# Optimization experiments

Hardware: AMD Instinct MI355X
Metric: run time of the kernel (lower is better)

Reference implementation:

```python
import jax, jax.numpy as jnp
import numpy as np

N = 50000      # nodes
E = 200000     # edges (before self-loops)
D_IN = 256
HID = 128
NEG_SLOPE = 0.2
BN_EPS = 1e-5


def _lin(k, fan_in, fan_out):
    return jax.random.normal(k, (fan_in, fan_out), jnp.float32) / np.float32(np.sqrt(fan_in))


def setup_inputs() -> dict:
    key = jax.random.key(0)
    ks = jax.random.split(key, 40)
    d = {}
    d['x'] = jax.random.normal(ks[0], (N, D_IN), jnp.float32)
    d['edge_index'] = jax.random.randint(ks[1], (2, E), 0, N, dtype=jnp.int32)
    # GAT layer 1: 256 -> 128, heads=4 (concat -> 512)
    d['W1'] = _lin(ks[2], D_IN, 4 * HID)
    d['asrc1'] = jax.random.normal(ks[3], (4, HID), jnp.float32) * 0.1
    d['adst1'] = jax.random.normal(ks[4], (4, HID), jnp.float32) * 0.1
    d['b1'] = jnp.zeros((4 * HID,), jnp.float32)
    d['g1'] = jax.random.uniform(ks[5], (4 * HID,), jnp.float32, 0.5, 1.5)
    d['be1'] = jax.random.normal(ks[6], (4 * HID,), jnp.float32) * 0.1
    d['m1'] = jax.random.normal(ks[7], (4 * HID,), jnp.float32) * 0.1
    d['v1'] = jax.random.uniform(ks[8], (4 * HID,), jnp.float32, 0.5, 1.5)
    # GAT layer 2: 512 -> 128, heads=4 (concat -> 512)
    d['W2'] = _lin(ks[9], 4 * HID, 4 * HID)
    d['asrc2'] = jax.random.normal(ks[10], (4, HID), jnp.float32) * 0.1
    d['adst2'] = jax.random.normal(ks[11], (4, HID), jnp.float32) * 0.1
    d['b2'] = jnp.zeros((4 * HID,), jnp.float32)
    d['g2'] = jax.random.uniform(ks[12], (4 * HID,), jnp.float32, 0.5, 1.5)
    d['be2'] = jax.random.normal(ks[13], (4 * HID,), jnp.float32) * 0.1
    d['m2'] = jax.random.normal(ks[14], (4 * HID,), jnp.float32) * 0.1
    d['v2'] = jax.random.uniform(ks[15], (4 * HID,), jnp.float32, 0.5, 1.5)
    # GAT layer 3: 512 -> 128, heads=1
    d['W3'] = _lin(ks[16], 4 * HID, HID)
    d['asrc3'] = jax.random.normal(ks[17], (1, HID), jnp.float32) * 0.1
    d['adst3'] = jax.random.normal(ks[18], (1, HID), jnp.float32) * 0.1
    d['b3'] = jnp.zeros((HID,), jnp.float32)
    d['g3'] = jax.random.uniform(ks[19], (HID,), jnp.float32, 0.5, 1.5)
    d['be3'] = jax.random.normal(ks[20], (HID,), jnp.float32) * 0.1
    d['m3'] = jax.random.normal(ks[21], (HID,), jnp.float32) * 0.1
    d['v3'] = jax.random.uniform(ks[22], (HID,), jnp.float32, 0.5, 1.5)
    # classifier head: 128 -> 64 -> 10
    d['Wc1'] = _lin(ks[23], HID, HID // 2)
    d['bc1'] = jnp.zeros((HID // 2,), jnp.float32)
    d['Wc2'] = _lin(ks[24], HID // 2, 10)
    d['bc2'] = jnp.zeros((10,), jnp.float32)
    return d


def _gat_layer(h, src, dst, W, asrc, adst, b, heads, ch):
    # PyG GATConv (eval mode): linear -> per-head scores -> segment softmax over dst -> aggregate
    xp = (h @ W).reshape(-1, heads, ch)                 # [N, H, C]
    e_src = (xp * asrc[None]).sum(-1)                   # [N, H]
    e_dst = (xp * adst[None]).sum(-1)                   # [N, H]
    e = jax.nn.leaky_relu(e_src[src] + e_dst[dst], NEG_SLOPE)  # [E', H]
    m = jax.lax.stop_gradient(jax.ops.segment_max(e, dst, num_segments=N))
    w = jnp.exp(e - m[dst])
    s = jax.ops.segment_sum(w, dst, num_segments=N)     # [N, H]
    alpha = w / (s[dst] + 1e-16)                        # [E', H]
    out = jax.ops.segment_sum(alpha[:, :, None] * xp[src], dst, num_segments=N)  # [N, H, C]
    return out.reshape(-1, heads * ch) + b


def _bn_relu(h, g, be, mu, var):
    return jax.nn.relu((h - mu) * jax.lax.rsqrt(var + BN_EPS) * g + be)


def reference(x, edge_index,
              W1, asrc1, adst1, b1, g1, be1, m1, v1,
              W2, asrc2, adst2, b2, g2, be2, m2, v2,
              W3, asrc3, adst3, b3, g3, be3, m3, v3,
              Wc1, bc1, Wc2, bc2):
    loop = jnp.arange(N, dtype=edge_index.dtype)
    src = jnp.concatenate([edge_index[0], loop])        # GATConv adds self-loops
    dst = jnp.concatenate([edge_index[1], loop])
    h = _bn_relu(_gat_layer(x, src, dst, W1, asrc1, adst1, b1, 4, HID), g1, be1, m1, v1)
    h = _bn_relu(_gat_layer(h, src, dst, W2, asrc2, adst2, b2, 4, HID), g2, be2, m2, v2)
    h = _bn_relu(_gat_layer(h, src, dst, W3, asrc3, adst3, b3, 1, HID), g3, be3, m3, v3)
    E_GNN = h                                           # [N, 128]
    logits = jax.nn.relu(E_GNN @ Wc1 + bc1) @ Wc2 + bc2 # [N, 10]
    P_GNN = jax.nn.softmax(logits, axis=-1)
    return (E_GNN, P_GNN)
```

## Files before the change

### kernel.cpp

```cpp
#include <hip/hip_runtime.h>
#include <math.h>

#define N_NODES 50000
#define N_EDGES 200000
#define NEG_SLOPE 0.2f
#define BN_EPS 1e-5f

#define SCAN_ELEMS 1024
#define SCAN_NB ((N_NODES + SCAN_ELEMS - 1) / SCAN_ELEMS)

typedef __attribute__((ext_vector_type(4))) float f32x4;
typedef __attribute__((ext_vector_type(8))) short bf16x8;
typedef __attribute__((ext_vector_type(8))) ushort u16x8;
typedef __attribute__((ext_vector_type(2))) ushort u16x2;

__device__ __forceinline__ ushort f2bf(float x) {
    unsigned u = __float_as_uint(x);
    u += 0x7FFFu + ((u >> 16) & 1u);
    return (ushort)(u >> 16);
}
__device__ __forceinline__ float bf2f(ushort u) {
    return __uint_as_float(((unsigned)u) << 16);
}

__global__ void k_init(int* cnt, int* off) {
    int i = blockIdx.x * blockDim.x + threadIdx.x;
    if (i < N_NODES) { cnt[i] = 1; off[i] = 1; }
}

__global__ void k_count(const int* __restrict__ ei, int* cnt) {
    int e = blockIdx.x * blockDim.x + threadIdx.x;
    if (e < N_EDGES) atomicAdd(&cnt[ei[N_EDGES + e]], 1);
}

__global__ __launch_bounds__(256) void k_scan1(const int* __restrict__ cnt,
                                               int* __restrict__ incl,
                                               int* __restrict__ partials) {
    __shared__ int sh[256];
    const int t = threadIdx.x;
    const int base = blockIdx.x * SCAN_ELEMS + t * 4;
    int v0 = 0, v1 = 0, v2 = 0, v3 = 0;
    if (base + 3 < N_NODES) {
        int4 lv = *reinterpret_cast<const int4*>(&cnt[base]);
        v0 = lv.x; v1 = lv.y; v2 = lv.z; v3 = lv.w;
    } else {
        if (base + 0 < N_NODES) v0 = cnt[base + 0];
        if (base + 1 < N_NODES) v1 = cnt[base + 1];
        if (base + 2 < N_NODES) v2 = cnt[base + 2];
        if (base + 3 < N_NODES) v3 = cnt[base + 3];
    }
    const int s1 = v0 + v1, s2 = s1 + v2, s3 = s2 + v3;
    sh[t] = s3;
    __syncthreads();
#pragma unroll
    for (int off = 1; off < 256; off <<= 1) {
        int x = (t >= off) ? sh[t - off] : 0;
        __syncthreads();
        sh[t] += x;
        __syncthreads();
    }
    const int excl = sh[t] - s3;
    if (base + 0 < N_NODES) incl[base + 0] = excl + v0;
    if (base + 1 < N_NODES) incl[base + 1] = excl + s1;
    if (base + 2 < N_NODES) incl[base + 2] = excl + s2;
    if (base + 3 < N_NODES) incl[base + 3] = excl + s3;
    if (t == 255) partials[blockIdx.x] = sh[255];
}

__global__ void k_scan2(const int* __restrict__ partials, int* __restrict__ pofs) {
    if (threadIdx.x == 0) {
        int s = 0;
        for (int b = 0; b < SCAN_NB; ++b) { pofs[b] = s; s += partials[b]; }
    }
}

__global__ void k_scan3(const int* __restrict__ incl, const int* __restrict__ pofs,
                        int* __restrict__ row_ptr) {
    int i = blockIdx.x * blockDim.x + threadIdx.x;
    if (i < N_NODES) row_ptr[i + 1] = incl[i] + pofs[i >> 10];
    if (i == 0) row_ptr[0] = 0;
}

__global__ void k_self(const int* __restrict__ row_ptr, int* colb) {
    int n = blockIdx.x * blockDim.x + threadIdx.x;
    if (n < N_NODES) colb[row_ptr[n]] = n;
}

__global__ void k_scatter(const int* __restrict__ ei, const int* __restrict__ row_ptr,
                          int* off, int* colb) {
    int e = blockIdx.x * blockDim.x + threadIdx.x;
    if (e < N_EDGES) {
        int dst = ei[N_EDGES + e];
        int p = atomicAdd(&off[dst], 1);
        colb[row_ptr[dst] + p] = ei[e];
    }
}

__global__ void k_cvt(const float* __restrict__ in, ushort* __restrict__ out, int n4) {
    int i = blockIdx.x * blockDim.x + threadIdx.x;
    if (i < n4) {
        float4 v = reinterpret_cast<const float4*>(in)[i];
        ushort4 o;
        o.x = f2bf(v.x); o.y = f2bf(v.y); o.z = f2bf(v.z); o.w = f2bf(v.w);
        reinterpret_cast<ushort4*>(out)[i] = o;
    }
}

__global__ void k_wt(const float* __restrict__ W, ushort* __restrict__ Wt, int K, int N) {
    int idx = blockIdx.x * blockDim.x + threadIdx.x;
    if (idx < K * N) {
        int n = idx / K, k = idx - n * K;
        Wt[idx] = f2bf(W[(size_t)k * N + n]);
    }
}

__global__ __launch_bounds__(512) void k_gemm256(const ushort* __restrict__ A,
                                                 const ushort* __restrict__ Bt,
                                                 ushort* __restrict__ Cb,
                                                 const float* __restrict__ asrc,
                                                 const float* __restrict__ adst,
                                                 float* __restrict__ es,
                                                 float* __restrict__ ed,
                                                 int M, int K) {
    constexpr int N = 512;
    __shared__ __align__(16) ushort As[128 * 32];
    __shared__ __align__(16) ushort Bs[256 * 32];
    __shared__ float sles[4][128];
    __shared__ float sled[4][128];
    const int tid = threadIdx.x;
    const int wid = tid >> 6, lane = tid & 63;
    const int wm = wid >> 2, wn = wid & 3;

    const int nwg = gridDim.x;
    const int q = nwg >> 3, r = nwg & 7;
    const int xcd = blockIdx.x & 7, bidx = blockIdx.x >> 3;
    const int wg = ((xcd < r) ? xcd * (q + 1) : r * (q + 1) + (xcd - r) * q) + bidx;
    const int row0 = (wg >> 1) * 128;
    const int by = wg & 1;
    const int col0 = by * 256;

    const int sub = lane >> 2;
    const int kcol = (lane & 3) * 8;

    const ushort* gPtr[3];
    ushort* lBase[3];
#pragma unroll
    for (int c = 0; c < 3; ++c) {
        int chunk = wid * 3 + c;
        if (chunk < 8) {
            int ar = row0 + chunk * 16 + sub;
            if (ar > M - 1) ar = M - 1;
            gPtr[c] = A + (size_t)ar * K + kcol;
            lBase[c] = As + chunk * 512;
        } else {
            int bc = chunk - 8;
            gPtr[c] = Bt + (size_t)(col0 + bc * 16 + sub) * K + kcol;
            lBase[c] = Bs + bc * 512;
        }
    }

    const int afr = (wm * 64 + (lane & 15)) * 32 + (lane >> 4) * 8;
    const int bfr = (wn * 64 + (lane & 15)) * 32 + (lane >> 4) * 8;

    f32x4 acc[4][4] = {};

    for (int k0 = 0; k0 < K; k0 += 32) {
#pragma unroll
        for (int c = 0; c < 3; ++c) {
            __builtin_amdgcn_global_load_lds(
                (const __attribute__((address_space(1))) unsigned*)(gPtr[c] + k0),
                (__attribute__((address_space(3))) unsigned*)lBase[c], 16, 0, 0);
        }
        __syncthreads();

        bf16x8 af[4], bg[4];
#pragma unroll
        for (int m = 0; m < 4; ++m)
            af[m] = *reinterpret_cast<const bf16x8*>(&As[afr + m * 16 * 32]);
#pragma unroll
        for (int n = 0; n < 4; ++n)
            bg[n] = *reinterpret_cast<const bf16x8*>(&Bs[bfr + n * 16 * 32]);
#pragma unroll
        for (int m = 0; m < 4; ++m)
#pragma unroll
            for (int n = 0; n < 4; ++n)
                acc[m][n] = __builtin_amdgcn_mfma_f32_16x16x32_bf16(af[m], bg[n], acc[m][n], 0, 0, 0);
        __syncthreads();
    }

    const int crow = row0 + wm * 64 + (lane >> 4) * 4;
    const int ccol = col0 + wn * 64 + (lane & 15);
#pragma unroll
    for (int m = 0; m < 4; ++m) {
#pragma unroll
        for (int j = 0; j < 4; ++j) {
            int rr = crow + m * 16 + j;
            if (rr < M) {
#pragma unroll
                for (int n = 0; n < 4; ++n)
                    Cb[(size_t)rr * N + ccol + n * 16] = f2bf(acc[m][n][j]);
            }
        }
    }

    const int head = by * 2 + (wn >> 1);
    float as_c[4], ad_c[4];
#pragma unroll
    for (int n = 0; n < 4; ++n) {
        int cl = (wn & 1) * 64 + n * 16 + (lane & 15);
        as_c[n] = asrc[head * 128 + cl];
        ad_c[n] = adst[head * 128 + cl];
    }
#pragma unroll
    for (int m = 0; m < 4; ++m) {
#pragma unroll
        for (int j = 0; j < 4; ++j) {
            float ps = acc[m][0][j] * as_c[0] + acc[m][1][j] * as_c[1] +
                       acc[m][2][j] * as_c[2] + acc[m][3][j] * as_c[3];
            float pd = acc[m][0][j] * ad_c[0] + acc[m][1][j] * ad_c[1] +
                       acc[m][2][j] * ad_c[2] + acc[m][3][j] * ad_c[3];
#pragma unroll
            for (int o = 1; o < 16; o <<= 1) {
                ps += __shfl_xor(ps, o);
                pd += __shfl_xor(pd, o);
            }
            if ((lane & 15) == 0) {
                int rl = wm * 64 + (lane >> 4) * 4 + m * 16 + j;
                sles[wn][rl] = ps;
                sled[wn][rl] = pd;
            }
        }
    }
    __syncthreads();
    if (tid < 256) {
        const int hl = tid >> 7;
        const int rl = tid & 127;
        const int rr = row0 + rl;
        if (rr < M) {
            es[(size_t)rr * 4 + by * 2 + hl] = sles[2 * hl][rl] + sles[2 * hl + 1][rl];
            ed[(size_t)rr * 4 + by * 2 + hl] = sled[2 * hl][rl] + sled[2 * hl + 1][rl];
        }
    }
}

__global__ __launch_bounds__(256) void k_gemm_bf16(const ushort* __restrict__ A,
                                                   const ushort* __restrict__ Bt,
                                                   ushort* __restrict__ Cb,
                                                   const float* __restrict__ asrc,
                                                   const float* __restrict__ adst,
                                                   float* __restrict__ es,
                                                   float* __restrict__ ed,
                                                   int M, int K, int N) {
    __shared__ __align__(16) ushort As[128 * 32];
    __shared__ __align__(16) ushort Bs[128 * 32];
    __shared__ float sles[2][128];
    __shared__ float sled[2][128];
    const int tid = threadIdx.x;
    const int wid = tid >> 6, lane = tid & 63;
    const int wm = wid >> 1, wn = wid & 1;
    const int row0 = blockIdx.x * 128, col0 = blockIdx.y * 128;
    const int H = N >> 7;

    const int c0 = wid * 2;
    const int sub = lane >> 2;
    const int kcol = (lane & 3) * 8;

    int ar0 = row0 + c0 * 16 + sub;      if (ar0 > M - 1) ar0 = M - 1;
    int ar1 = row0 + c0 * 16 + 16 + sub; if (ar1 > M - 1) ar1 = M - 1;
    const size_t gA0 = (size_t)ar0 * K + kcol;
    const size_t gA1 = (size_t)ar1 * K + kcol;
    const size_t gB0 = (size_t)(col0 + c0 * 16 + sub) * K + kcol;
    const size_t gB1 = gB0 + (size_t)16 * K;
    ushort* lA0 = As + c0 * 512;
    ushort* lA1 = lA0 + 512;
    ushort* lB0 = Bs + c0 * 512;
    ushort* lB1 = lB0 + 512;

    const int afr = (wm * 64 + (lane & 15)) * 32 + (lane >> 4) * 8;
    const int bfr = (wn * 64 + (lane & 15)) * 32 + (lane >> 4) * 8;

    f32x4 acc[4][4] = {};

    for (int k0 = 0; k0 < K; k0 += 32) {
        __builtin_amdgcn_global_load_lds(
            (const __attribute__((address_space(1))) unsigned*)(A + gA0 + k0),
            (__attribute__((address_space(3))) unsigned*)lA0, 16, 0, 0);
        __builtin_amdgcn_global_load_lds(
            (const __attribute__((address_space(1))) unsigned*)(A + gA1 + k0),
            (__attribute__((address_space(3))) unsigned*)lA1, 16, 0, 0);
        __builtin_amdgcn_global_load_lds(
            (const __attribute__((address_space(1))) unsigned*)(Bt + gB0 + k0),
            (__attribute__((address_space(3))) unsigned*)lB0, 16, 0, 0);
        __builtin_amdgcn_global_load_lds(
            (const __attribute__((address_space(1))) unsigned*)(Bt + gB1 + k0),
            (__attribute__((address_space(3))) unsigned*)lB1, 16, 0, 0);
        __syncthreads();

        bf16x8 af[4], bg[4];
#pragma unroll
        for (int m = 0; m < 4; ++m)
            af[m] = *reinterpret_cast<const bf16x8*>(&As[afr + m * 16 * 32]);
#pragma unroll
        for (int n = 0; n < 4; ++n)
            bg[n] = *reinterpret_cast<const bf16x8*>(&Bs[bfr + n * 16 * 32]);
#pragma unroll
        for (int m = 0; m < 4; ++m)
#pragma unroll
            for (int n = 0; n < 4; ++n)
                acc[m][n] = __builtin_amdgcn_mfma_f32_16x16x32_bf16(af[m], bg[n], acc[m][n], 0, 0, 0);
        __syncthreads();
    }

    const int crow = row0 + wm * 64 + (lane >> 4) * 4;
    const int ccol = col0 + wn * 64 + (lane & 15);
#pragma unroll
    for (int m = 0; m < 4; ++m) {
#pragma unroll
        for (int j = 0; j < 4; ++j) {
            int r = crow + m * 16 + j;
            if (r < M) {
#pragma unroll
                for (int n = 0; n < 4; ++n)
                    Cb[(size_t)r * N + ccol + n * 16] = f2bf(acc[m][n][j]);
            }
        }
    }

    float as_c[4], ad_c[4];
#pragma unroll
    for (int n = 0; n < 4; ++n) {
        int cl = wn * 64 + n * 16 + (lane & 15);
        as_c[n] = asrc[blockIdx.y * 128 + cl];
        ad_c[n] = adst[blockIdx.y * 128 + cl];
    }
#pragma unroll
    for (int m = 0; m < 4; ++m) {
#pragma unroll
        for (int j = 0; j < 4; ++j) {
            float ps = acc[m][0][j] * as_c[0] + acc[m][1][j] * as_c[1] +
                       acc[m][2][j] * as_c[2] + acc[m][3][j] * as_c[3];
            float pd = acc[m][0][j] * ad_c[0] + acc[m][1][j] * ad_c[1] +
                       acc[m][2][j] * ad_c[2] + acc[m][3][j] * ad_c[3];
#pragma unroll
            for (int o = 1; o < 16; o <<= 1) {
                ps += __shfl_xor(ps, o);
                pd += __shfl_xor(pd, o);
            }
            if ((lane & 15) == 0) {
                int rl = wm * 64 + (lane >> 4) * 4 + m * 16 + j;
                sles[wn][rl] = ps;
                sled[wn][rl] = pd;
            }
        }
    }
    __syncthreads();
    if (tid < 128) {
        int r = row0 + tid;
        if (r < M) {
            es[(size_t)r * H + blockIdx.y] = sles[0][tid] + sles[1][tid];
            ed[(size_t)r * H + blockIdx.y] = sled[0][tid] + sled[1][tid];
        }
    }
}

template <int H, bool BF16OUT>
__global__ __launch_bounds__(64) void k_agg(
    const ushort* __restrict__ xpb, const float* __restrict__ es, const float* __restrict__ ed,
    const int* __restrict__ row_ptr, const int* __restrict__ colb,
    const float* __restrict__ bias, const float* __restrict__ gg, const float* __restrict__ be,
    const float* __restrict__ mu, const float* __restrict__ var, void* __restrict__ outv) {
    constexpr int HC = H * 128;
    constexpr int CPT = HC / 64;
    constexpr int CHUNK = 128;
    constexpr int GS = (H == 4) ? 16 : 64;
    __shared__ int s_src[CHUNK];
    __shared__ float s_w[CHUNK][H];
    const int n = blockIdx.x;
    const int lane = threadIdx.x;
    const int g = (H == 4) ? (lane >> 4) : 0;
    const int gl = (H == 4) ? (lane & 15) : lane;
    const int beg = row_ptr[n], end = row_ptr[n + 1];
    const int cnt = end - beg;

    float edn[H];
#pragma unroll
    for (int h = 0; h < H; ++h) edn[h] = ed[n * H + h];

    float acc[CPT];
#pragma unroll
    for (int j = 0; j < CPT; ++j) acc[j] = 0.f;
    float m_run = -INFINITY, s_run = 0.f;
    const int ch0 = lane * CPT;
    const ushort* xb = xpb + ch0;

    for (int cbeg = 0; cbeg < cnt; cbeg += CHUNK) {
        const int cc = min(cnt - cbeg, CHUNK);
        for (int i = lane; i < cc; i += 64) {
            int src = colb[beg + cbeg + i];
            s_src[i] = src;
            if (H == 4) {
                float4 e4 = *reinterpret_cast<const float4*>(&es[src * 4]);
                float4 o;
                o.x = e4.x + edn[0]; o.x = (o.x > 0.f) ? o.x : NEG_SLOPE * o.x;
                o.y = e4.y + edn[1]; o.y = (o.y > 0.f) ? o.y : NEG_SLOPE * o.y;
                o.z = e4.z + edn[2]; o.z = (o.z > 0.f) ? o.z : NEG_SLOPE * o.z;
                o.w = e4.w + edn[3]; o.w = (o.w > 0.f) ? o.w : NEG_SLOPE * o.w;
                *reinterpret_cast<float4*>(&s_w[i][0]) = o;
            } else {
                float e = es[src] + edn[0];
                s_w[i][0] = (e > 0.f) ? e : NEG_SLOPE * e;
            }
        }
        __syncthreads();
        float cm = -INFINITY;
        for (int i = gl; i < cc; i += GS) cm = fmaxf(cm, s_w[i][g]);
#pragma unroll
        for (int o = GS >> 1; o; o >>= 1) cm = fmaxf(cm, __shfl_xor(cm, o));
        const float m_new = fmaxf(m_run, cm);
        const float scale = __expf(m_run - m_new);
        float sl = 0.f;
        for (int i = gl; i < cc; i += GS) {
            float w = __expf(s_w[i][g] - m_new);
            s_w[i][g] = w;
            sl += w;
        }
#pragma unroll
        for (int o = GS >> 1; o; o >>= 1) sl += __shfl_xor(sl, o);
        s_run = s_run * scale + sl;
        m_run = m_new;
#pragma unroll
        for (int j = 0; j < CPT; ++j) acc[j] *= scale;
        __syncthreads();
        for (int e = 0; e < cc; e += 4) {
            float w0 = s_w[e][g];
            int   p0 = s_src[e];
            float w1 = 0.f; int p1 = n;
            float w2 = 0.f; int p2 = n;
            float w3 = 0.f; int p3 = n;
            if (e + 1 < cc) { w1 = s_w[e + 1][g]; p1 = s_src[e + 1]; }
            if (e + 2 < cc) { w2 = s_w[e + 2][g]; p2 = s_src[e + 2]; }
            if (e + 3 < cc) { w3 = s_w[e + 3][g]; p3 = s_src[e + 3]; }
            if (CPT == 8) {
                u16x8 v0 = *reinterpret_cast<const u16x8*>(xb + (size_t)p0 * HC);
                u16x8 v1 = *reinterpret_cast<const u16x8*>(xb + (size_t)p1 * HC);
                u16x8 v2 = *reinterpret_cast<const u16x8*>(xb + (size_t)p2 * HC);
                u16x8 v3 = *reinterpret_cast<const u16x8*>(xb + (size_t)p3 * HC);
#pragma unroll
                for (int j = 0; j < CPT; ++j) {
                    float a = acc[j];
                    a = fmaf(w0, bf2f(v0[j]), a);
                    a = fmaf(w1, bf2f(v1[j]), a);
                    a = fmaf(w2, bf2f(v2[j]), a);
                    a = fmaf(w3, bf2f(v3[j]), a);
                    acc[j] = a;
                }
            } else {
                u16x2 v0 = *reinterpret_cast<const u16x2*>(xb + (size_t)p0 * HC);
                u16x2 v1 = *reinterpret_cast<const u16x2*>(xb + (size_t)p1 * HC);
                u16x2 v2 = *reinterpret_cast<const u16x2*>(xb + (size_t)p2 * HC);
                u16x2 v3 = *reinterpret_cast<const u16x2*>(xb + (size_t)p3 * HC);
#pragma unroll
                for (int j = 0; j < CPT; ++j) {
                    float a = acc[j];
                    a = fmaf(w0, bf2f(v0[j]), a);
                    a = fmaf(w1, bf2f(v1[j]), a);
                    a = fmaf(w2, bf2f(v2[j]), a);
                    a = fmaf(w3, bf2f(v3[j]), a);
                    acc[j] = a;
                }
            }
        }
        __syncthreads();
    }

    const float inv = 1.f / (s_run + 1e-16f);
    float vals[CPT];
#pragma unroll
    for (int j = 0; j < CPT; ++j) {
        int ch = ch0 + j;
        float val = acc[j] * inv + bias[ch];
        val = (val - mu[ch]) * (gg[ch] * rsqrtf(var[ch] + BN_EPS)) + be[ch];
        vals[j] = fmaxf(val, 0.f);
    }
    if (BF16OUT) {
        if (CPT == 8) {
            u16x8 o;
#pragma unroll
            for (int j = 0; j < CPT; ++j) o[j] = f2bf(vals[j]);
            *reinterpret_cast<u16x8*>((ushort*)outv + (size_t)n * HC + ch0) = o;
        } else {
            u16x2 o;
#pragma unroll
            for (int j = 0; j < CPT; ++j) o[j] = f2bf(vals[j]);
            *reinterpret_cast<u16x2*>((ushort*)outv + (size_t)n * HC + ch0) = o;
        }
    } else {
        float2 o = make_float2(vals[0], vals[1 % CPT]);
        *reinterpret_cast<float2*>((float*)outv + (size_t)n * HC + ch0) = o;
    }
}

#define CLS_NB 16
__global__ __launch_bounds__(256) void k_cls(const float* __restrict__ Eg,
                                             const float* __restrict__ Wc1,
                                             const float* __restrict__ bc1,
                                             const float* __restrict__ Wc2,
                                             const float* __restrict__ bc2,
                                             float* __restrict__ P) {
    __shared__ float Ws[128 * 64];
    __shared__ float W2s[64 * 10 + 16];
    __shared__ float b1s[64];
    __shared__ float e_sh[CLS_NB][128];
    __shared__ float h_sh[CLS_NB][64];
    __shared__ float l_sh[CLS_NB][10];
    const int t = threadIdx.x;
    const int n0 = blockIdx.x * CLS_NB;

    for (int i = t; i < 2048; i += 256)
        reinterpret_cast<float4*>(Ws)[i] = reinterpret_cast<const float4*>(Wc1)[i];
    for (int i = t; i < 640; i += 256) W2s[i] = Wc2[i];
    if (t < 64) b1s[t] = bc1[t];
    if (t >= 64 && t < 74) W2s[640 + t - 64] = bc2[t - 64];
    for (int i = t; i < CLS_NB * 32; i += 256) {
        int node = i >> 5, qq = i & 31;
        reinterpret_cast<float4*>(&e_sh[node][0])[qq] =
            reinterpret_cast<const float4*>(&Eg[(size_t)(n0 + node) * 128])[qq];
    }
    __syncthreads();

    {
        const int c = t & 63, ng = t >> 6;
        float acc0 = b1s[c], acc1 = b1s[c], acc2 = b1s[c], acc3 = b1s[c];
        for (int k = 0; k < 128; ++k) {
            float w = Ws[k * 64 + c];
            acc0 = fmaf(e_sh[ng * 4 + 0][k], w, acc0);
            acc1 = fmaf(e_sh[ng * 4 + 1][k], w, acc1);
            acc2 = fmaf(e_sh[ng * 4 + 2][k], w, acc2);
            acc3 = fmaf(e_sh[ng * 4 + 3][k], w, acc3);
        }
        h_sh[ng * 4 + 0][c] = fmaxf(acc0, 0.f);
        h_sh[ng * 4 + 1][c] = fmaxf(acc1, 0.f);
        h_sh[ng * 4 + 2][c] = fmaxf(acc2, 0.f);
        h_sh[ng * 4 + 3][c] = fmaxf(acc3, 0.f);
    }
    __syncthreads();
    if (t < CLS_NB * 10) {
        int node = t / 10, c = t - node * 10;
        float acc = W2s[640 + c];
        for (int k = 0; k < 64; ++k) acc = fmaf(h_sh[node][k], W2s[k * 10 + c], acc);
        l_sh[node][c] = acc;
    }
    __syncthreads();
    if (t < CLS_NB) {
        float mx = l_sh[t][0];
        for (int j = 1; j < 10; ++j) mx = fmaxf(mx, l_sh[t][j]);
        float s = 0.f;
        float ex[10];
        for (int j = 0; j < 10; ++j) { ex[j] = __expf(l_sh[t][j] - mx); s += ex[j]; }
        float inv = 1.f / s;
        for (int j = 0; j < 10; ++j) l_sh[t][j] = ex[j] * inv;
    }
    __syncthreads();
    if (t < CLS_NB * 10) {
        int node = t / 10, c = t - node * 10;
        P[(size_t)(n0 + node) * 10 + c] = l_sh[node][c];
    }
}

extern "C" void kernel_launch(void* const* d_in, const int* in_sizes, int n_in,
                              void* d_out, int out_size, void* d_ws, size_t ws_size,
                              hipStream_t stream) {
    const float* x     = (const float*)d_in[0];
    const int*   ei    = (const int*)d_in[1];
    const float* W1    = (const float*)d_in[2];
    const float* asrc1 = (const float*)d_in[3];
    const float* adst1 = (const float*)d_in[4];
    const float* b1    = (const float*)d_in[5];
    const float* gg1   = (const float*)d_in[6];
    const float* be1   = (const float*)d_in[7];
    const float* mu1   = (const float*)d_in[8];
    const float* v1    = (const float*)d_in[9];
    const float* W2    = (const float*)d_in[10];
    const float* asrc2 = (const float*)d_in[11];
    const float* adst2 = (const float*)d_in[12];
    const float* b2    = (const float*)d_in[13];
    const float* gg2   = (const float*)d_in[14];
    const float* be2   = (const float*)d_in[15];
    const float* mu2   = (const float*)d_in[16];
    const float* v2    = (const float*)d_in[17];
    const float* W3    = (const float*)d_in[18];
    const float* asrc3 = (const float*)d_in[19];
    const float* adst3 = (const float*)d_in[20];
    const float* b3    = (const float*)d_in[21];
    const float* gg3   = (const float*)d_in[22];
    const float* be3   = (const float*)d_in[23];
    const float* mu3   = (const float*)d_in[24];
    const float* v3    = (const float*)d_in[25];
    const float* Wc1   = (const float*)d_in[26];
    const float* bc1   = (const float*)d_in[27];
    const float* Wc2   = (const float*)d_in[28];
    const float* bc2   = (const float*)d_in[29];

    ushort* xpb  = (ushort*)d_ws;
    ushort* hh   = xpb + (size_t)N_NODES * 512;
    ushort* wt1  = hh + (size_t)N_NODES * 512;
    ushort* wt2  = wt1 + 512 * 256;
    ushort* wt3  = wt2 + 512 * 512;
    float*  es   = (float*)(wt3 + 128 * 512);
    float*  ed   = es + (size_t)N_NODES * 4;
    int* cnt     = (int*)(ed + (size_t)N_NODES * 4);
    int* off     = cnt + N_NODES;
    int* row_ptr = off + N_NODES;
    int* colb    = row_ptr + N_NODES + 4;
    int* incl    = colb + N_EDGES + N_NODES;
    int* partials = incl + N_NODES;
    int* pofs    = partials + SCAN_NB;

    float* Egnn = (float*)d_out;
    float* P    = Egnn + (size_t)N_NODES * 128;

    k_init<<<(N_NODES + 255) / 256, 256, 0, stream>>>(cnt, off);
    k_count<<<(N_EDGES + 255) / 256, 256, 0, stream>>>(ei, cnt);
    k_scan1<<<SCAN_NB, 256, 0, stream>>>(cnt, incl, partials);
    k_scan2<<<1, 64, 0, stream>>>(partials, pofs);
    k_scan3<<<(N_NODES + 255) / 256, 256, 0, stream>>>(incl, pofs, row_ptr);
    k_self<<<(N_NODES + 255) / 256, 256, 0, stream>>>(row_ptr, colb);
    k_scatter<<<(N_EDGES + 255) / 256, 256, 0, stream>>>(ei, row_ptr, off, colb);

    k_wt<<<(512 * 256 + 255) / 256, 256, 0, stream>>>(W1, wt1, 256, 512);
    k_wt<<<(512 * 512 + 255) / 256, 256, 0, stream>>>(W2, wt2, 512, 512);
    k_wt<<<(128 * 512 + 255) / 256, 256, 0, stream>>>(W3, wt3, 512, 128);
    {
        int n4 = N_NODES * 256 / 4;
        k_cvt<<<(n4 + 255) / 256, 256, 0, stream>>>(x, hh, n4);
    }

    const int mt = (N_NODES + 127) / 128;
    const int nwg256 = mt * 2;

    k_gemm256<<<nwg256, 512, 0, stream>>>(hh, wt1, xpb, asrc1, adst1, es, ed,
                                          N_NODES, 256);
    k_agg<4, true><<<N_NODES, 64, 0, stream>>>(xpb, es, ed, row_ptr, colb,
                                               b1, gg1, be1, mu1, v1, hh);
    k_gemm256<<<nwg256, 512, 0, stream>>>(hh, wt2, xpb, asrc2, adst2, es, ed,
                                          N_NODES, 512);
    k_agg<4, true><<<N_NODES, 64, 0, stream>>>(xpb, es, ed, row_ptr, colb,
                                               b2, gg2, be2, mu2, v2, hh);
    {
        dim3 grid(mt, 1);
        k_gemm_bf16<<<grid, 256, 0, stream>>>(hh, wt3, xpb, asrc3, adst3, es, ed,
                                              N_NODES, 512, 128);
    }
    k_agg<1, false><<<N_NODES, 64, 0, stream>>>(xpb, es, ed, row_ptr, colb,
                                                b3, gg3, be3, mu3, v3, Egnn);
    k_cls<<<(N_NODES + CLS_NB - 1) / CLS_NB, 256, 0, stream>>>(Egnn, Wc1, bc1, Wc2, bc2, P);
}
```

Baseline: 451.6 us.

## Double-buffer LDS tiles in both bf16 GEMM kernels to overlap loads with MFMA

Both GEMM kernels now keep two LDS buffers and prefetch the next K-slice with global_load_lds while MFMAs run on the current slice. This drops one barrier per iteration and is meant to hide global-load latency behind compute. In exchange LDS use doubles, which can lower occupancy. Correctness depends on the single barrier per iteration also waiting for the async LDS writes to finish.

```diff
diff --git a/kernel.cpp b/kernel.cpp
--- a/kernel.cpp
+++ b/kernel.cpp
@@ -123,8 +123,7 @@
                                                  float* __restrict__ ed,
                                                  int M, int K) {
     constexpr int N = 512;
-    __shared__ __align__(16) ushort As[128 * 32];
-    __shared__ __align__(16) ushort Bs[256 * 32];
+    __shared__ __align__(16) ushort L[2][12288];
     __shared__ float sles[4][128];
     __shared__ float sled[4][128];
     const int tid = threadIdx.x;
@@ -143,49 +142,70 @@
     const int kcol = (lane & 3) * 8;
 
     const ushort* gPtr[3];
-    ushort* lBase[3];
+    int lOfs[3];
 #pragma unroll
     for (int c = 0; c < 3; ++c) {
         int chunk = wid * 3 + c;
+        lOfs[c] = chunk * 512;
         if (chunk < 8) {
             int ar = row0 + chunk * 16 + sub;
             if (ar > M - 1) ar = M - 1;
             gPtr[c] = A + (size_t)ar * K + kcol;
-            lBase[c] = As + chunk * 512;
         } else {
             int bc = chunk - 8;
             gPtr[c] = Bt + (size_t)(col0 + bc * 16 + sub) * K + kcol;
-            lBase[c] = Bs + bc * 512;
         }
     }
 
     const int afr = (wm * 64 + (lane & 15)) * 32 + (lane >> 4) * 8;
-    const int bfr = (wn * 64 + (lane & 15)) * 32 + (lane >> 4) * 8;
+    const int bfr = 4096 + (wn * 64 + (lane & 15)) * 32 + (lane >> 4) * 8;
 
     f32x4 acc[4][4] = {};
 
-    for (int k0 = 0; k0 < K; k0 += 32) {
-#pragma unroll
-        for (int c = 0; c < 3; ++c) {
+#pragma unroll
+    for (int c = 0; c < 3; ++c)
+        __builtin_amdgcn_global_load_lds(
+            (const __attribute__((address_space(1))) unsigned*)(gPtr[c]),
+            (__attribute__((address_space(3))) unsigned*)(&L[0][lOfs[c]]), 16, 0, 0);
+    __syncthreads();
+
+    int cur = 0;
+    for (int k0 = 32; k0 < K; k0 += 32) {
+#pragma unroll
+        for (int c = 0; c < 3; ++c)
             __builtin_amdgcn_global_load_lds(
                 (const __attribute__((address_space(1))) unsigned*)(gPtr[c] + k0),
-                (__attribute__((address_space(3))) unsigned*)lBase[c], 16, 0, 0);
+                (__attribute__((address_space(3))) unsigned*)(&L[cur ^ 1][lOfs[c]]), 16, 0, 0);
+        {
+            bf16x8 af[4], bg[4];
+#pragma unroll
+            for (int m = 0; m < 4; ++m)
+                af[m] = *reinterpret_cast<const bf16x8*>(&L[cur][afr + m * 16 * 32]);
+#pragma unroll
+            for (int n = 0; n < 4; ++n)
+                bg[n] = *reinterpret_cast<const bf16x8*>(&L[cur][bfr + n * 16 * 32]);
+#pragma unroll
+            for (int m = 0; m < 4; ++m)
+#pragma unroll
+                for (int n = 0; n < 4; ++n)
+                    acc[m][n] = __builtin_amdgcn_mfma_f32_16x16x32_bf16(af[m], bg[n], acc[m][n], 0, 0, 0);
         }
         __syncthreads();
-
+        cur ^= 1;
+    }
+    {
         bf16x8 af[4], bg[4];
 #pragma unroll
         for (int m = 0; m < 4; ++m)
-            af[m] = *reinterpret_cast<const bf16x8*>(&As[afr + m * 16 * 32]);
+            af[m] = *reinterpret_cast<const bf16x8*>(&L[cur][afr + m * 16 * 32]);
 #pragma unroll
         for (int n = 0; n < 4; ++n)
-            bg[n] = *reinterpret_cast<const bf16x8*>(&Bs[bfr + n * 16 * 32]);
+            bg[n] = *reinterpret_cast<const bf16x8*>(&L[cur][bfr + n * 16 * 32]);
 #pragma unroll
         for (int m = 0; m < 4; ++m)
 #pragma unroll
             for (int n = 0; n < 4; ++n)
                 acc[m][n] = __builtin_amdgcn_mfma_f32_16x16x32_bf16(af[m], bg[n], acc[m][n], 0, 0, 0);
-        __syncthreads();
     }
 
     const int crow = row0 + wm * 64 + (lane >> 4) * 4;
@@ -251,8 +271,7 @@
                                                    float* __restrict__ es,
                                                    float* __restrict__ ed,
                                                    int M, int K, int N) {
-    __shared__ __align__(16) ushort As[128 * 32];
-    __shared__ __align__(16) ushort Bs[128 * 32];
+    __shared__ __align__(16) ushort L[2][8192];
     __shared__ float sles[2][128];
     __shared__ float sled[2][128];
     const int tid = threadIdx.x;
@@ -261,54 +280,74 @@
     const int row0 = blockIdx.x * 128, col0 = blockIdx.y * 128;
     const int H = N >> 7;
 
-    const int c0 = wid * 2;
     const int sub = lane >> 2;
     const int kcol = (lane & 3) * 8;
 
-    int ar0 = row0 + c0 * 16 + sub;      if (ar0 > M - 1) ar0 = M - 1;
-    int ar1 = row0 + c0 * 16 + 16 + sub; if (ar1 > M - 1) ar1 = M - 1;
-    const size_t gA0 = (size_t)ar0 * K + kcol;
-    const size_t gA1 = (size_t)ar1 * K + kcol;
-    const size_t gB0 = (size_t)(col0 + c0 * 16 + sub) * K + kcol;
-    const size_t gB1 = gB0 + (size_t)16 * K;
-    ushort* lA0 = As + c0 * 512;
-    ushort* lA1 = lA0 + 512;
-    ushort* lB0 = Bs + c0 * 512;
-    ushort* lB1 = lB0 + 512;
+    const ushort* gPtr[4];
+    int lOfs[4];
+#pragma unroll
+    for (int c = 0; c < 4; ++c) {
+        int chunk = wid * 4 + c;
+        lOfs[c] = chunk * 512;
+        if (chunk < 8) {
+            int ar = row0 + chunk * 16 + sub;
+            if (ar > M - 1) ar = M - 1;
+            gPtr[c] = A + (size_t)ar * K + kcol;
+        } else {
+            int bc = chunk - 8;
+            gPtr[c] = Bt + (size_t)(col0 + bc * 16 + sub) * K + kcol;
+        }
+    }
 
     const int afr = (wm * 64 + (lane & 15)) * 32 + (lane >> 4) * 8;
-    const int bfr = (wn * 64 + (lane & 15)) * 32 + (lane >> 4) * 8;
+    const int bfr = 4096 + (wn * 64 + (lane & 15)) * 32 + (lane >> 4) * 8;
 
     f32x4 acc[4][4] = {};
 
-    for (int k0 = 0; k0 < K; k0 += 32) {
+#pragma unroll
+    for (int c = 0; c < 4; ++c)
         __builtin_amdgcn_global_load_lds(
-            (const __attribute__((address_space(1))) unsigned*)(A + gA0 + k0),
-            (__attribute__((address_space(3))) unsigned*)lA0, 16, 0, 0);
-        __builtin_amdgcn_global_load_lds(
-            (const __attribute__((address_space(1))) unsigned*)(A + gA1 + k0),
-            (__attribute__((address_space(3))) unsigned*)lA1, 16, 0, 0);
-        __builtin_amdgcn_global_load_lds(
-            (const __attribute__((address_space(1))) unsigned*)(Bt + gB0 + k0),
-            (__attribute__((address_space(3))) unsigned*)lB0, 16, 0, 0);
-        __builtin_amdgcn_global_load_lds(
-            (const __attribute__((address_space(1))) unsigned*)(Bt + gB1 + k0),
-            (__attribute__((address_space(3))) unsigned*)lB1, 16, 0, 0);
+            (const __attribute__((address_space(1))) unsigned*)(gPtr[c]),
+            (__attribute__((address_space(3))) unsigned*)(&L[0][lOfs[c]]), 16, 0, 0);
+    __syncthreads();
+
+    int cur = 0;
+    for (int k0 = 32; k0 < K; k0 += 32) {
+#pragma unroll
+        for (int c = 0; c < 4; ++c)
+            __builtin_amdgcn_global_load_lds(
+                (const __attribute__((address_space(1))) unsigned*)(gPtr[c] + k0),
+                (__attribute__((address_space(3))) unsigned*)(&L[cur ^ 1][lOfs[c]]), 16, 0, 0);
+        {
+            bf16x8 af[4], bg[4];
+#pragma unroll
+            for (int m = 0; m < 4; ++m)
+                af[m] = *reinterpret_cast<const bf16x8*>(&L[cur][afr + m * 16 * 32]);
+#pragma unroll
+            for (int n = 0; n < 4; ++n)
+                bg[n] = *reinterpret_cast<const bf16x8*>(&L[cur][bfr + n * 16 * 32]);
+#pragma unroll
+            for (int m = 0; m < 4; ++m)
+#pragma unroll
+                for (int n = 0; n < 4; ++n)
+                    acc[m][n] = __builtin_amdgcn_mfma_f32_16x16x32_bf16(af[m], bg[n], acc[m][n], 0, 0, 0);
+        }
         __syncthreads();
-
+        cur ^= 1;
+    }
+    {
         bf16x8 af[4], bg[4];
 #pragma unroll
         for (int m = 0; m < 4; ++m)
-            af[m] = *reinterpret_cast<const bf16x8*>(&As[afr + m * 16 * 32]);
+            af[m] = *reinterpret_cast<const bf16x8*>(&L[cur][afr + m * 16 * 32]);
 #pragma unroll
         for (int n = 0; n < 4; ++n)
-            bg[n] = *reinterpret_cast<const bf16x8*>(&Bs[bfr + n * 16 * 32]);
+            bg[n] = *reinterpret_cast<const bf16x8*>(&L[cur][bfr + n * 16 * 32]);
 #pragma unroll
         for (int m = 0; m < 4; ++m)
 #pragma unroll
             for (int n = 0; n < 4; ++n)
                 acc[m][n] = __builtin_amdgcn_mfma_f32_16x16x32_bf16(af[m], bg[n], acc[m][n], 0, 0, 0);
-        __syncthreads();
     }
 
     const int crow = row0 + wm * 64 + (lane >> 4) * 4;
```

Result: no change. 446.0 us (-1.2%).
